# Optimization experiments

Hardware: AMD Instinct MI355X
Metric: run time of the kernel (lower is better)

The kernel has to match this reference:

```python
import jax, jax.numpy as jnp
import numpy as np

WINDOW_SIZE = 7
SIGMA = 1.5


def _gaussian_window(size, sigma, channel):
    coords = jnp.arange(size, dtype=jnp.float32) - size // 2
    g = jnp.exp(-coords ** 2 / (2.0 * sigma ** 2))
    g = g / g.sum()
    g3d = g[:, None, None] * g[None, :, None] * g[None, None, :]  # [k,k,k]
    # depthwise kernel: [out_ch=channel, in_ch/groups=1, kD, kH, kW]
    return jnp.broadcast_to(g3d[None, None], (channel, 1, size, size, size))


def _depthwise_conv3d(x, window):
    ch = x.shape[1]
    return jax.lax.conv_general_dilated(
        x, window,
        window_strides=(1, 1, 1),
        padding='SAME',
        dimension_numbers=('NCDHW', 'OIDHW', 'NCDHW'),
        feature_group_count=ch,
    )


def setup_inputs() -> dict:
    key = jax.random.key(0)
    k1, k2 = jax.random.split(key)
    shape = (4, 1, 160, 160, 160)
    prediction = jax.random.uniform(k1, shape, dtype=jnp.float32)
    target = jax.random.uniform(k2, shape, dtype=jnp.float32)
    return {"prediction": prediction, "target": target}


def reference(prediction, target):
    C1 = 0.01 ** 2
    C2 = 0.03 ** 2
    ch = prediction.shape[1]
    window = _gaussian_window(WINDOW_SIZE, SIGMA, ch).astype(prediction.dtype)

    mu_pred = _depthwise_conv3d(prediction, window)
    mu_tgt = _depthwise_conv3d(target, window)
    mu_pred_sq = mu_pred ** 2
    mu_tgt_sq = mu_tgt ** 2
    mu_cross = mu_pred * mu_tgt

    sigma_pred_sq = _depthwise_conv3d(prediction ** 2, window) - mu_pred_sq
    sigma_tgt_sq = _depthwise_conv3d(target ** 2, window) - mu_tgt_sq
    sigma_cross = _depthwise_conv3d(prediction * target, window) - mu_cross

    ssim_map = ((2.0 * mu_cross + C1) * (2.0 * sigma_cross + C2)) / (
        (mu_pred_sq + mu_tgt_sq + C1) * (sigma_pred_sq + sigma_tgt_sq + C2))
    return 1.0 - ssim_map.mean()
```

## Files before the change

### kernel.cpp

```cpp
#include <hip/hip_runtime.h>
#include <hip/hip_fp16.h>

#define DIM   160
#define DIM2  25600
#define TY    32
#define TX    32
#define TZ    16
#define HY    38
#define HX    38
#define SS    51
#define NSL   22
#define NSITE (HY * HX)
#define NVOX_D 16384000.0

#define W0 0.03663285f
#define W1 0.11128076f
#define W2 0.21674532f
#define W3 0.27068213f

__global__ void ssim_zero_acc(double* acc) {
    if (threadIdx.x == 0 && blockIdx.x == 0) acc[0] = 0.0;
}

__global__ __launch_bounds__(256, 3) void ssim_main(const float* __restrict__ P,
                                                    const float* __restrict__ T,
                                                    double* __restrict__ acc) {
    const float Wf[7] = {W0, W1, W2, W3, W2, W1, W0};
    const __half2 wh[7] = {__float2half2_rn(W0), __float2half2_rn(W1),
                           __float2half2_rn(W2), __float2half2_rn(W3),
                           __float2half2_rn(W2), __float2half2_rn(W1),
                           __float2half2_rn(W0)};

    __shared__ __half2 sIn[HY * SS];
    __shared__ __half2 ycMu[TY * SS];
    __shared__ __half2 ycE2[TY * SS];
    __shared__ float   ycPt[TY * SS];
    __shared__ float   red[4];

    const int tid = threadIdx.x;
    int bid = blockIdx.x;
    int b  = bid / 250;  int r  = bid - b * 250;
    int zc = r / 25;     int r2 = r - zc * 25;
    int ty = r2 / 5;     int tx = r2 - ty * 5;

    const int base = b * (DIM * DIM * DIM);
    const int z0 = zc * TZ, y0 = ty * TY - 3, x0 = tx * TX - 3;

    int gofs[6], lofs[6];
    bool ld[6], st[6];
#pragma unroll
    for (int k = 0; k < 6; ++k) {
        int u = tid + 256 * k;
        st[k] = (u < NSITE);
        int y = u / HX, x = u - y * HX;
        int gy = y0 + y, gx = x0 + x;
        ld[k] = st[k] & ((unsigned)gy < (unsigned)DIM) & ((unsigned)gx < (unsigned)DIM);
        gofs[k] = gy * DIM + gx;
        lofs[k] = y * SS + x;
    }

    int yb[3];
#pragma unroll
    for (int q = 0; q < 3; ++q) {
        int t = tid + 256 * q; if (t > 607) t = 607;
        int yy = t / HX, x = t - yy * HX;
        yb[q] = (2 * yy) * SS + x;
    }

    const int xrd = (tid >> 3) * SS + 4 * (tid & 7);

    const __half2 hz = __float2half2_rn(0.f);
    __half2 azMu[4][7], azE2[4][7], azPtA[7], azPtB[7];
#pragma unroll
    for (int o = 0; o < 4; ++o)
#pragma unroll
        for (int j = 0; j < 7; ++j) { azMu[o][j] = hz; azE2[o][j] = hz; }
#pragma unroll
    for (int j = 0; j < 7; ++j) { azPtA[j] = hz; azPtB[j] = hz; }

    float lsum = 0.f;

    auto ytask = [&](int ybase) {
        __half2 mu0 = hz, mu1 = hz, e20 = hz, e21 = hz;
        float pt0 = 0.f, pt1 = 0.f;
#pragma unroll
        for (int k = 0; k < 8; ++k) {
            __half2 v  = sIn[ybase + k * SS];
            __half2 v2 = __hmul2(v, v);
            __half2 vs = __halves2half2(__high2half(v), __low2half(v));
            float ptf  = __low2float(__hmul2(v, vs));
            if (k < 7) {
                mu0 = __hfma2(wh[k], v, mu0);
                e20 = __hfma2(wh[k], v2, e20);
                pt0 = fmaf(Wf[k], ptf, pt0);
            }
            if (k >= 1) {
                mu1 = __hfma2(wh[k - 1], v, mu1);
                e21 = __hfma2(wh[k - 1], v2, e21);
                pt1 = fmaf(Wf[k - 1], ptf, pt1);
            }
        }
        ycMu[ybase] = mu0; ycMu[ybase + SS] = mu1;
        ycE2[ybase] = e20; ycE2[ybase + SS] = e21;
        ycPt[ybase] = pt0; ycPt[ybase + SS] = pt1;
    };

    {
        int zs = z0 - 3;
        bool zok = (unsigned)zs < (unsigned)DIM;
        const float* Pp = P + base + zs * DIM2;
        const float* Tp = T + base + zs * DIM2;
        float rp[6], rt[6];
#pragma unroll
        for (int k = 0; k < 6; ++k) {
            rp[k] = 0.f; rt[k] = 0.f;
            if (zok && ld[k]) { rp[k] = Pp[gofs[k]]; rt[k] = Tp[gofs[k]]; }
        }
#pragma unroll
        for (int k = 0; k < 6; ++k)
            if (st[k]) sIn[lofs[k]] = __floats2half2_rn(rp[k], rt[k]);
    }
    __syncthreads();

    for (int i = 0; i < NSL; ++i) {
        const bool hn = (i + 1 < NSL);
        float rp[6], rt[6];

        if (hn) {
            int zs = z0 + i - 2;
            bool zok = (unsigned)zs < (unsigned)DIM;
            const float* Pp = P + base + zs * DIM2;
            const float* Tp = T + base + zs * DIM2;
#pragma unroll
            for (int k = 0; k < 6; ++k) {
                rp[k] = 0.f; rt[k] = 0.f;
                if (zok && ld[k]) { rp[k] = Pp[gofs[k]]; rt[k] = Tp[gofs[k]]; }
            }
        }

        ytask(yb[0]);
        ytask(yb[1]);
        if (tid < 96) ytask(yb[2]);
        __syncthreads();

        __half2 muw[10], e2w[10]; float ptw[10];
#pragma unroll
        for (int m = 0; m < 10; ++m) {
            muw[m] = ycMu[xrd + m];
            e2w[m] = ycE2[xrd + m];
            ptw[m] = ycPt[xrd + m];
        }
        __half2 xmu[4], xe2[4]; float xpt[4];
#pragma unroll
        for (int o = 0; o < 4; ++o) {
            __half2 am = hz, ae = hz; float ap = 0.f;
#pragma unroll
            for (int k = 0; k < 7; ++k) {
                am = __hfma2(wh[k], muw[o + k], am);
                ae = __hfma2(wh[k], e2w[o + k], ae);
                ap = fmaf(Wf[k], ptw[o + k], ap);
            }
            xmu[o] = am; xe2[o] = ae; xpt[o] = ap;
        }

        __half2 ptA = __floats2half2_rn(xpt[0], xpt[1]);
        __half2 ptB = __floats2half2_rn(xpt[2], xpt[3]);
#pragma unroll
        for (int j = 0; j < 7; ++j) {
            __half2 w2 = wh[6 - j];
#pragma unroll
            for (int o = 0; o < 4; ++o) {
                azMu[o][j] = __hfma2(w2, xmu[o], azMu[o][j]);
                azE2[o][j] = __hfma2(w2, xe2[o], azE2[o][j]);
            }
            azPtA[j] = __hfma2(w2, ptA, azPtA[j]);
            azPtB[j] = __hfma2(w2, ptB, azPtB[j]);
        }

        if (i >= 6) {
            float eptv[4] = {__low2float(azPtA[0]), __high2float(azPtA[0]),
                             __low2float(azPtB[0]), __high2float(azPtB[0])};
#pragma unroll
            for (int o = 0; o < 4; ++o) {
                float mp = __low2float(azMu[o][0]), mt = __high2float(azMu[o][0]);
                float ep2 = __low2float(azE2[o][0]), et2 = __high2float(azE2[o][0]);
                float mp2 = mp * mp, mt2 = mt * mt, mpt = mp * mt;
                float num = fmaf(2.f, mpt, 1e-4f) * fmaf(2.f, eptv[o] - mpt, 9e-4f);
                float den = (mp2 + mt2 + 1e-4f) * ((ep2 - mp2) + (et2 - mt2) + 9e-4f);
                lsum += num * __builtin_amdgcn_rcpf(den);
            }
        }

#pragma unroll
        for (int j = 0; j < 6; ++j) {
#pragma unroll
            for (int o = 0; o < 4; ++o) {
                azMu[o][j] = azMu[o][j + 1];
                azE2[o][j] = azE2[o][j + 1];
            }
            azPtA[j] = azPtA[j + 1];
            azPtB[j] = azPtB[j + 1];
        }
#pragma unroll
        for (int o = 0; o < 4; ++o) { azMu[o][6] = hz; azE2[o][6] = hz; }
        azPtA[6] = hz; azPtB[6] = hz;

        if (hn) {
#pragma unroll
            for (int k = 0; k < 6; ++k)
                if (st[k]) sIn[lofs[k]] = __floats2half2_rn(rp[k], rt[k]);
        }
        __syncthreads();
    }

#pragma unroll
    for (int off = 32; off > 0; off >>= 1) lsum += __shfl_down(lsum, off);
    if ((tid & 63) == 0) red[tid >> 6] = lsum;
    __syncthreads();
    if (tid == 0) atomicAdd(acc, (double)(red[0] + red[1] + red[2] + red[3]));
}

__global__ void ssim_finalize(const double* __restrict__ acc, float* __restrict__ out) {
    if (threadIdx.x == 0 && blockIdx.x == 0)
        out[0] = 1.f - (float)(acc[0] / NVOX_D);
}

extern "C" void kernel_launch(void* const* d_in, const int* in_sizes, int n_in,
                              void* d_out, int out_size, void* d_ws, size_t ws_size,
                              hipStream_t stream) {
    const float* P = (const float*)d_in[0];
    const float* T = (const float*)d_in[1];
    float* out = (float*)d_out;
    double* acc = (double*)d_ws;

    ssim_zero_acc<<<1, 64, 0, stream>>>(acc);
    ssim_main<<<4 * 10 * 5 * 5, 256, 0, stream>>>(P, T, acc);
    ssim_finalize<<<1, 64, 0, stream>>>(acc, out);
}
```

Baseline: 102.6 us.

## Rotate z-accumulator ring by unrolled phase, shrink cross-term LDS to fp16, raise occupancy

Replaces the per-slice shift of the 7-deep z accumulator registers with a ring buffer whose index is a compile-time phase, unrolling the slice loop by seven so no register moves are needed. The y-pass cross-product buffer in shared memory is stored as fp16 instead of fp32, shrinking LDS use. Launch bounds now request four blocks per SIMD instead of three. The fp16 cross term reduces precision, and the larger unrolled body plus the tighter register budget may cause spills.

```diff
diff --git a/kernel.cpp b/kernel.cpp
--- a/kernel.cpp
+++ b/kernel.cpp
@@ -1,5 +1,6 @@
 #include <hip/hip_runtime.h>
 #include <hip/hip_fp16.h>
+#include <type_traits>
 
 #define DIM   160
 #define DIM2  25600
@@ -22,7 +23,7 @@
     if (threadIdx.x == 0 && blockIdx.x == 0) acc[0] = 0.0;
 }
 
-__global__ __launch_bounds__(256, 3) void ssim_main(const float* __restrict__ P,
+__global__ __launch_bounds__(256, 4) void ssim_main(const float* __restrict__ P,
                                                     const float* __restrict__ T,
                                                     double* __restrict__ acc) {
     const float Wf[7] = {W0, W1, W2, W3, W2, W1, W0};
@@ -34,7 +35,7 @@
     __shared__ __half2 sIn[HY * SS];
     __shared__ __half2 ycMu[TY * SS];
     __shared__ __half2 ycE2[TY * SS];
-    __shared__ float   ycPt[TY * SS];
+    __shared__ __half  ycPt[TY * SS];
     __shared__ float   red[4];
 
     const int tid = threadIdx.x;
@@ -102,7 +103,7 @@
         }
         ycMu[ybase] = mu0; ycMu[ybase + SS] = mu1;
         ycE2[ybase] = e20; ycE2[ybase + SS] = e21;
-        ycPt[ybase] = pt0; ycPt[ybase + SS] = pt1;
+        ycPt[ybase] = __float2half(pt0); ycPt[ybase + SS] = __float2half(pt1);
     };
 
     {
@@ -122,7 +123,8 @@
     }
     __syncthreads();
 
-    for (int i = 0; i < NSL; ++i) {
+    auto body = [&](auto phc, int i) {
+        constexpr int PH = decltype(phc)::value;
         const bool hn = (i + 1 < NSL);
         float rp[6], rt[6];
 
@@ -148,7 +150,7 @@
         for (int m = 0; m < 10; ++m) {
             muw[m] = ycMu[xrd + m];
             e2w[m] = ycE2[xrd + m];
-            ptw[m] = ycPt[xrd + m];
+            ptw[m] = __half2float(ycPt[xrd + m]);
         }
         __half2 xmu[4], xe2[4]; float xpt[4];
 #pragma unroll
@@ -167,23 +169,25 @@
         __half2 ptB = __floats2half2_rn(xpt[2], xpt[3]);
 #pragma unroll
         for (int j = 0; j < 7; ++j) {
+            constexpr int JS[7] = {0, 1, 2, 3, 4, 5, 6};
+            const int s = (JS[j] + PH) % 7;
             __half2 w2 = wh[6 - j];
 #pragma unroll
             for (int o = 0; o < 4; ++o) {
-                azMu[o][j] = __hfma2(w2, xmu[o], azMu[o][j]);
-                azE2[o][j] = __hfma2(w2, xe2[o], azE2[o][j]);
-            }
-            azPtA[j] = __hfma2(w2, ptA, azPtA[j]);
-            azPtB[j] = __hfma2(w2, ptB, azPtB[j]);
+                azMu[o][s] = __hfma2(w2, xmu[o], azMu[o][s]);
+                azE2[o][s] = __hfma2(w2, xe2[o], azE2[o][s]);
+            }
+            azPtA[s] = __hfma2(w2, ptA, azPtA[s]);
+            azPtB[s] = __hfma2(w2, ptB, azPtB[s]);
         }
 
         if (i >= 6) {
-            float eptv[4] = {__low2float(azPtA[0]), __high2float(azPtA[0]),
-                             __low2float(azPtB[0]), __high2float(azPtB[0])};
+            float eptv[4] = {__low2float(azPtA[PH]), __high2float(azPtA[PH]),
+                             __low2float(azPtB[PH]), __high2float(azPtB[PH])};
 #pragma unroll
             for (int o = 0; o < 4; ++o) {
-                float mp = __low2float(azMu[o][0]), mt = __high2float(azMu[o][0]);
-                float ep2 = __low2float(azE2[o][0]), et2 = __high2float(azE2[o][0]);
+                float mp = __low2float(azMu[o][PH]), mt = __high2float(azMu[o][PH]);
+                float ep2 = __low2float(azE2[o][PH]), et2 = __high2float(azE2[o][PH]);
                 float mp2 = mp * mp, mt2 = mt * mt, mpt = mp * mt;
                 float num = fmaf(2.f, mpt, 1e-4f) * fmaf(2.f, eptv[o] - mpt, 9e-4f);
                 float den = (mp2 + mt2 + 1e-4f) * ((ep2 - mp2) + (et2 - mt2) + 9e-4f);
@@ -192,18 +196,8 @@
         }
 
 #pragma unroll
-        for (int j = 0; j < 6; ++j) {
-#pragma unroll
-            for (int o = 0; o < 4; ++o) {
-                azMu[o][j] = azMu[o][j + 1];
-                azE2[o][j] = azE2[o][j + 1];
-            }
-            azPtA[j] = azPtA[j + 1];
-            azPtB[j] = azPtB[j + 1];
-        }
-#pragma unroll
-        for (int o = 0; o < 4; ++o) { azMu[o][6] = hz; azE2[o][6] = hz; }
-        azPtA[6] = hz; azPtB[6] = hz;
+        for (int o = 0; o < 4; ++o) { azMu[o][PH] = hz; azE2[o][PH] = hz; }
+        azPtA[PH] = hz; azPtB[PH] = hz;
 
         if (hn) {
 #pragma unroll
@@ -211,7 +205,19 @@
                 if (st[k]) sIn[lofs[k]] = __floats2half2_rn(rp[k], rt[k]);
         }
         __syncthreads();
-    }
+    };
+
+#pragma unroll 1
+    for (int ib = 0; ib < 21; ib += 7) {
+        body(std::integral_constant<int, 0>{}, ib + 0);
+        body(std::integral_constant<int, 1>{}, ib + 1);
+        body(std::integral_constant<int, 2>{}, ib + 2);
+        body(std::integral_constant<int, 3>{}, ib + 3);
+        body(std::integral_constant<int, 4>{}, ib + 4);
+        body(std::integral_constant<int, 5>{}, ib + 5);
+        body(std::integral_constant<int, 6>{}, ib + 6);
+    }
+    body(std::integral_constant<int, 0>{}, 21);
 
 #pragma unroll
     for (int off = 32; off > 0; off >>= 1) lsum += __shfl_down(lsum, off);
```

Measured after the change: 188.8 us. 1.84x slower.

## Double-buffer shared slices to drop one barrier per z-step and store cross term as half

Applied to the files above, without the earlier changes.

Shared input and y-pass buffers become ping-pong pairs. The next slice is written into the alternate buffer before the single barrier, so the second __syncthreads per iteration goes away. The y-filtered cross-product plane is stored as half instead of float to keep the extra shared memory in check. This adds LDS footprint, which may reduce occupancy, and lowers precision on the cross term.

```diff
diff --git a/kernel.cpp b/kernel.cpp
--- a/kernel.cpp
+++ b/kernel.cpp
@@ -31,10 +31,10 @@
                            __float2half2_rn(W2), __float2half2_rn(W1),
                            __float2half2_rn(W0)};
 
-    __shared__ __half2 sIn[HY * SS];
-    __shared__ __half2 ycMu[TY * SS];
-    __shared__ __half2 ycE2[TY * SS];
-    __shared__ float   ycPt[TY * SS];
+    __shared__ __half2 sIn[2][HY * SS];
+    __shared__ __half2 ycMu[2][TY * SS];
+    __shared__ __half2 ycE2[2][TY * SS];
+    __shared__ __half  ycPt[2][TY * SS];
     __shared__ float   red[4];
 
     const int tid = threadIdx.x;
@@ -80,12 +80,12 @@
 
     float lsum = 0.f;
 
-    auto ytask = [&](int ybase) {
+    auto ytask = [&](const __half2* si, __half2* mu_, __half2* e2_, __half* pt_, int ybase) {
         __half2 mu0 = hz, mu1 = hz, e20 = hz, e21 = hz;
         float pt0 = 0.f, pt1 = 0.f;
 #pragma unroll
         for (int k = 0; k < 8; ++k) {
-            __half2 v  = sIn[ybase + k * SS];
+            __half2 v  = si[ybase + k * SS];
             __half2 v2 = __hmul2(v, v);
             __half2 vs = __halves2half2(__high2half(v), __low2half(v));
             float ptf  = __low2float(__hmul2(v, vs));
@@ -100,55 +100,56 @@
                 pt1 = fmaf(Wf[k - 1], ptf, pt1);
             }
         }
-        ycMu[ybase] = mu0; ycMu[ybase + SS] = mu1;
-        ycE2[ybase] = e20; ycE2[ybase + SS] = e21;
-        ycPt[ybase] = pt0; ycPt[ybase + SS] = pt1;
+        mu_[ybase] = mu0; mu_[ybase + SS] = mu1;
+        e2_[ybase] = e20; e2_[ybase + SS] = e21;
+        pt_[ybase] = __float2half(pt0); pt_[ybase + SS] = __float2half(pt1);
     };
 
-    {
-        int zs = z0 - 3;
+    float rp[6], rt[6];
+    auto prefetch = [&](int i) {
+        int zs = z0 - 3 + i;
         bool zok = (unsigned)zs < (unsigned)DIM;
         const float* Pp = P + base + zs * DIM2;
         const float* Tp = T + base + zs * DIM2;
-        float rp[6], rt[6];
 #pragma unroll
         for (int k = 0; k < 6; ++k) {
             rp[k] = 0.f; rt[k] = 0.f;
             if (zok && ld[k]) { rp[k] = Pp[gofs[k]]; rt[k] = Tp[gofs[k]]; }
         }
-#pragma unroll
-        for (int k = 0; k < 6; ++k)
-            if (st[k]) sIn[lofs[k]] = __floats2half2_rn(rp[k], rt[k]);
-    }
+    };
+
+    prefetch(0);
+#pragma unroll
+    for (int k = 0; k < 6; ++k)
+        if (st[k]) sIn[0][lofs[k]] = __floats2half2_rn(rp[k], rt[k]);
     __syncthreads();
 
+    int cur = 0;
     for (int i = 0; i < NSL; ++i) {
         const bool hn = (i + 1 < NSL);
-        float rp[6], rt[6];
+
+        if (hn) prefetch(i + 1);
+
+        ytask(sIn[cur], ycMu[cur], ycE2[cur], ycPt[cur], yb[0]);
+        ytask(sIn[cur], ycMu[cur], ycE2[cur], ycPt[cur], yb[1]);
+        if (tid < 96) ytask(sIn[cur], ycMu[cur], ycE2[cur], ycPt[cur], yb[2]);
 
         if (hn) {
-            int zs = z0 + i - 2;
-            bool zok = (unsigned)zs < (unsigned)DIM;
-            const float* Pp = P + base + zs * DIM2;
-            const float* Tp = T + base + zs * DIM2;
-#pragma unroll
-            for (int k = 0; k < 6; ++k) {
-                rp[k] = 0.f; rt[k] = 0.f;
-                if (zok && ld[k]) { rp[k] = Pp[gofs[k]]; rt[k] = Tp[gofs[k]]; }
-            }
-        }
-
-        ytask(yb[0]);
-        ytask(yb[1]);
-        if (tid < 96) ytask(yb[2]);
+#pragma unroll
+            for (int k = 0; k < 6; ++k)
+                if (st[k]) sIn[cur ^ 1][lofs[k]] = __floats2half2_rn(rp[k], rt[k]);
+        }
         __syncthreads();
 
+        const __half2* mu_ = ycMu[cur];
+        const __half2* e2_ = ycE2[cur];
+        const __half*  pt_ = ycPt[cur];
         __half2 muw[10], e2w[10]; float ptw[10];
 #pragma unroll
         for (int m = 0; m < 10; ++m) {
-            muw[m] = ycMu[xrd + m];
-            e2w[m] = ycE2[xrd + m];
-            ptw[m] = ycPt[xrd + m];
+            muw[m] = mu_[xrd + m];
+            e2w[m] = e2_[xrd + m];
+            ptw[m] = __half2float(pt_[xrd + m]);
         }
         __half2 xmu[4], xe2[4]; float xpt[4];
 #pragma unroll
@@ -205,12 +206,7 @@
         for (int o = 0; o < 4; ++o) { azMu[o][6] = hz; azE2[o][6] = hz; }
         azPtA[6] = hz; azPtB[6] = hz;
 
-        if (hn) {
-#pragma unroll
-            for (int k = 0; k < 6; ++k)
-                if (st[k]) sIn[lofs[k]] = __floats2half2_rn(rp[k], rt[k]);
-        }
-        __syncthreads();
+        cur ^= 1;
     }
 
 #pragma unroll
```

Measured after the change: 143.1 us. +39.5%, slower.
